# Kernel tuning notes

Measured on AMD Instinct MI355X. Metric: run time of the kernel, lower is better.

## Reference

```python
import jax, jax.numpy as jnp
import numpy as np

B, S, D = 2, 4096, 1024
H, HD = 16, 64
M = 512              # memseqlen == chunk size
L = 2 * M            # memory + chunk tokens
HID = 2816
EPS = 1e-5


def setup_inputs() -> dict:
    key = jax.random.key(0)
    ks = jax.random.split(key, 16)
    sc = 0.02
    return {
        "x": jax.random.normal(ks[0], (B, S, D), jnp.float32),
        "freqs_cos": jax.random.uniform(ks[1], (L, HD // 2), jnp.float32),
        "freqs_sin": jax.random.uniform(ks[2], (L, HD // 2), jnp.float32),
        "wq": jax.random.normal(ks[3], (D, D), jnp.float32) * sc,
        "wk": jax.random.normal(ks[4], (D, D), jnp.float32) * sc,
        "wv": jax.random.normal(ks[5], (D, D), jnp.float32) * sc,
        "wo": jax.random.normal(ks[6], (D, D), jnp.float32) * sc,
        "wm": jax.random.normal(ks[7], (D, D), jnp.float32) * sc,
        "wkm": jax.random.normal(ks[8], (D, D), jnp.float32) * sc,
        "wvm": jax.random.normal(ks[9], (D, D), jnp.float32) * sc,
        "w1": jax.random.normal(ks[10], (D, HID), jnp.float32) * sc,
        "w3": jax.random.normal(ks[11], (D, HID), jnp.float32) * sc,
        "w2": jax.random.normal(ks[12], (HID, D), jnp.float32) * sc,
        "ffn_norm_w": jnp.ones((D,), jnp.float32),
        "mem_norm_w": jnp.ones((D,), jnp.float32),
        "origin_mem": jnp.zeros((1, M, D), jnp.float32),
    }


def _rmsnorm(x, w):
    return x * jax.lax.rsqrt(jnp.mean(x * x, axis=-1, keepdims=True) + EPS) * w


def _rope(t, cos, sin):
    # t: (B, L, H, HD); cos/sin: (L, HD//2). Adjacent-pair complex rotation (llama2.c style).
    tr = t.reshape(*t.shape[:-1], HD // 2, 2)
    t_r, t_i = tr[..., 0], tr[..., 1]
    c = cos[None, :, None, :]
    s = sin[None, :, None, :]
    o_r = t_r * c - t_i * s
    o_i = t_r * s + t_i * c
    return jnp.stack([o_r, o_i], axis=-1).reshape(t.shape)


def reference(x, freqs_cos, freqs_sin, wq, wk, wv, wo, wm, wkm, wvm,
              w1, w2, w3, ffn_norm_w, mem_norm_w, origin_mem):
    bsz = x.shape[0]
    cos = freqs_cos[:L]
    sin = freqs_sin[:L]
    causal = jnp.tril(jnp.ones((L, L), dtype=bool))
    scale = 1.0 / jnp.sqrt(jnp.asarray(HD, x.dtype))

    def ffn(h):
        return (jax.nn.silu(h @ w1) * (h @ w3)) @ w2

    def step(om, subx):
        # token projections
        xq = (subx @ wq).reshape(bsz, M, H, HD)
        xk = (subx @ wk).reshape(bsz, M, H, HD)
        xv = (subx @ wv).reshape(bsz, M, H, HD)
        # memory glue: wm -> ffn residual -> rmsnorm
        om2 = om @ wm
        om2 = om2 + ffn(_rmsnorm(om2, ffn_norm_w))
        om2 = _rmsnorm(om2, mem_norm_w)
        # memory projections (source bug: mq is overwritten by mk; wqm unused)
        mk = (om2 @ wkm).reshape(bsz, M, H, HD)
        mv = (om2 @ wvm).reshape(bsz, M, H, HD)
        mq = mk
        q = jnp.concatenate([mq, xq], axis=1)  # (B, L, H, HD)
        k = jnp.concatenate([mk, xk], axis=1)
        v = jnp.concatenate([mv, xv], axis=1)
        q = _rope(q, cos, sin)
        k = _rope(k, cos, sin)
        # SDPA, causal over the concatenated length (n_rep == 1, repeat_kv is identity)
        qh = q.transpose(0, 2, 1, 3)
        kh = k.transpose(0, 2, 1, 3)
        vh = v.transpose(0, 2, 1, 3)
        scores = jnp.einsum('bhqd,bhkd->bhqk', qh, kh) * scale
        scores = jnp.where(causal, scores, jnp.finfo(scores.dtype).min)
        attn = jax.nn.softmax(scores, axis=-1)
        out = jnp.einsum('bhqk,bhkd->bhqd', attn, vh)
        out = out.transpose(0, 2, 1, 3).reshape(bsz, L, D)
        om_new = out[:, M:]  # token-part becomes next memory AND this chunk's output
        return om_new, om_new

    om0 = jnp.broadcast_to(origin_mem, (bsz, M, D))
    xc = x.reshape(bsz, S // M, M, D).transpose(1, 0, 2, 3)  # (n_chunks, B, M, D)
    _, outs = jax.lax.scan(step, om0, xc)
    out = outs.transpose(1, 0, 2, 3).reshape(bsz, S, D)
    return out @ wo
```

## Files before the change

kernel.cpp:

```cpp
#include <hip/hip_runtime.h>
#include <hip/hip_bf16.h>


#define D_    1024
#define H_    16
#define HD_   64
#define M_    512
#define L_    1024
#define HID_  2816
#define NSTEP 8

typedef __hip_bfloat16 bf16;
typedef _Float16 f16;
typedef __attribute__((ext_vector_type(8))) short short8;
typedef __attribute__((ext_vector_type(8))) _Float16 f16x8;
typedef __attribute__((ext_vector_type(4))) _Float16 f16x4;
typedef __attribute__((ext_vector_type(2))) _Float16 f16x2;
typedef __attribute__((ext_vector_type(4))) float floatx4;

__global__ void probe_dtype(const void* x, int* flag) {
  int lane = threadIdx.x;
  unsigned short v = ((const unsigned short*)x)[2 * lane];
  int e = (v >> 7) & 0xFF;
  bool sane = (e >= 100 && e <= 140);
  unsigned long long m = __ballot(sane);
  if (lane == 0) flag[0] = (__popcll(m) >= 40) ? 1 : 0;
}

__device__ __forceinline__ float load_any(const void* p, long i, int isbf) {
  return isbf ? __bfloat162float(((const bf16*)p)[i]) : ((const float*)p)[i];
}

__global__ __launch_bounds__(256) void transpose_cast(const void* in, bf16* out,
                                                      int K, int N, const int* flagp,
                                                      int stride, int off) {
  __shared__ float tile[32][33];
  int isbf = flagp[0];
  int tx = threadIdx.x & 31, ty = threadIdx.x >> 5;
  int n = blockIdx.x * 32 + tx;
#pragma unroll
  for (int i = 0; i < 4; i++) {
    int k = blockIdx.y * 32 + ty + i * 8;
    tile[ty + i * 8][tx] = load_any(in, (long)k * N + n, isbf);
  }
  __syncthreads();
  int k2 = blockIdx.y * 32 + tx;
#pragma unroll
  for (int i = 0; i < 4; i++) {
    int n2 = blockIdx.x * 32 + ty + i * 8;
    out[((long)n2 * stride + off) * K + k2] = __float2bfloat16(tile[tx][ty + i * 8]);
  }
}

__global__ __launch_bounds__(256) void cast_to_bf16(const void* in, bf16* out, int n,
                                                    const int* flagp) {
  int i = blockIdx.x * 256 + threadIdx.x;
  if (i < n) out[i] = __float2bfloat16(load_any(in, i, flagp[0]));
}

__global__ __launch_bounds__(256) void cast_to_f32(const void* in, float* out, int n,
                                                   const int* flagp) {
  int i = blockIdx.x * 256 + threadIdx.x;
  if (i < n) out[i] = load_any(in, i, flagp[0]);
}

__global__ __launch_bounds__(256) void init_om(const void* in, bf16* om, const int* flagp) {
  int i = blockIdx.x * 256 + threadIdx.x;
  int rem = i & (M_ * D_ - 1);
  om[i] = __float2bfloat16(load_any(in, rem, flagp[0]));
}

#define GEMM64_BODY(Aptr, WTptr, Kld, kbeg, kend)                                   \
  __shared__ char smem[16384];                                                      \
  char* aT = smem;                                                                  \
  char* bT = smem + 8192;                                                           \
  int tid = threadIdx.x;                                                            \
  int wave = tid >> 6, lane = tid & 63;                                             \
  int wm_ = wave >> 1, wn_ = wave & 1;                                              \
  floatx4 acc[2][2] = {};                                                           \
  int q0 = tid, q1 = tid + 256;                                                     \
  int am0 = q0 >> 3, ac0 = q0 & 7;                                                  \
  int am1 = q1 >> 3, ac1 = q1 & 7;                                                  \
  long grow0 = R0 + am0, grow1 = R0 + am1;                                          \
  long bn0 = (long)(C0 + am0) * (Kld), bn1 = (long)(C0 + am1) * (Kld);              \
  int lofa0 = (am0 * 8 + (ac0 ^ (am0 & 7))) * 16;                                   \
  int lofa1 = (am1 * 8 + (ac1 ^ (am1 & 7))) * 16;                                   \
  for (int k0 = (kbeg); k0 < (kend); k0 += 64) {                                    \
    uint4 va0 = *(const uint4*)((Aptr) + grow0 * (Kld) + k0 + ac0 * 8);             \
    uint4 va1 = *(const uint4*)((Aptr) + grow1 * (Kld) + k0 + ac1 * 8);             \
    uint4 vb0 = *(const uint4*)((WTptr) + bn0 + k0 + ac0 * 8);                      \
    uint4 vb1 = *(const uint4*)((WTptr) + bn1 + k0 + ac1 * 8);                      \
    __syncthreads();                                                                \
    *(uint4*)(aT + lofa0) = va0;                                                    \
    *(uint4*)(aT + lofa1) = va1;                                                    \
    *(uint4*)(bT + lofa0) = vb0;                                                    \
    *(uint4*)(bT + lofa1) = vb1;                                                    \
    __syncthreads();                                                                \
    _Pragma("unroll") for (int kki = 0; kki < 2; ++kki) {                           \
      int cbase = kki * 4 + (lane >> 4);                                            \
      short8 af[2], bfr[2];                                                         \
      _Pragma("unroll") for (int i = 0; i < 2; ++i) {                               \
        int ml = wm_ * 32 + i * 16 + (lane & 15);                                   \
        af[i] = *(const short8*)(aT + (ml * 8 + (cbase ^ (ml & 7))) * 16);          \
        int nl = wn_ * 32 + i * 16 + (lane & 15);                                   \
        bfr[i] = *(const short8*)(bT + (nl * 8 + (cbase ^ (nl & 7))) * 16);         \
      }                                                                             \
      _Pragma("unroll") for (int i = 0; i < 2; ++i)                                 \
          _Pragma("unroll") for (int j = 0; j < 2; ++j) acc[i][j] =                 \
              __builtin_amdgcn_mfma_f32_16x16x32_bf16(af[i], bfr[j], acc[i][j],     \
                                                      0, 0, 0);                     \
    }                                                                               \
  }

__global__ __launch_bounds__(256) void gemm64_sk(
    const bf16* __restrict__ A, const bf16* __restrict__ WT,
    float* __restrict__ outP, int N, int Kfull, int Ksplit) {
  int C0 = blockIdx.x * 64, R0 = blockIdx.y * 64;
  int kb = blockIdx.z;
  float* out = outP + ((size_t)kb << 20);
  int kbeg = kb * Ksplit;
  GEMM64_BODY(A, WT, Kfull, kbeg, kbeg + Ksplit)
#pragma unroll
  for (int i = 0; i < 2; ++i)
#pragma unroll
    for (int j = 0; j < 2; ++j) {
      int row = R0 + wm_ * 32 + i * 16 + (lane >> 4) * 4;
      int col = C0 + wn_ * 32 + j * 16 + (lane & 15);
#pragma unroll
      for (int rg = 0; rg < 4; ++rg)
        out[(long)(row + rg) * N + col] = acc[i][j][rg];
    }
}

__global__ __launch_bounds__(256) void gemm64_kmvm(
    const bf16* __restrict__ A, const bf16* __restrict__ WT,
    const float* __restrict__ cosf, const float* __restrict__ sinf,
    f16* __restrict__ k_mem, f16* __restrict__ v_memT) {
  int C0 = blockIdx.x * 64, R0 = blockIdx.y * 64;
  GEMM64_BODY(A, WT, 1024, 0, 1024)
#pragma unroll
  for (int i = 0; i < 2; ++i)
#pragma unroll
    for (int j = 0; j < 2; ++j) {
      int row0 = R0 + wm_ * 32 + i * 16 + (lane >> 4) * 4;
      int col = C0 + wn_ * 32 + j * 16 + (lane & 15);
#pragma unroll
      for (int rg = 0; rg < 4; ++rg) {
        float v = acc[i][j][rg];
        int row = row0 + rg;
        int b = row >> 9, pos = row & 511;
        if (C0 < 1024) {
          float partner = __shfl_xor(v, 1);
          int ii = (col & 63) >> 1;
          float c = cosf[pos * 32 + ii], s = sinf[pos * 32 + ii];
          float o = (col & 1) ? (partner * s + v * c) : (v * c - partner * s);
          int bh = b * 16 + ((col >> 6) & 15);
          k_mem[((size_t)bh * 512 + pos) * 64 + (col & 63)] = (f16)o;
        } else {
          int d = col & 63;
          int bh = b * 16 + ((col - 1024) >> 6);
          v_memT[((size_t)bh * 64 + d) * 512 + pos] = (f16)v;
        }
      }
    }
}

__global__ __launch_bounds__(256) void gemm128(
    const bf16* __restrict__ A, const bf16* __restrict__ WT,
    void* __restrict__ out, const int* __restrict__ flagp,
    int N, int K, int out_mode,
    const float* __restrict__ cosf, const float* __restrict__ sinf,
    f16* __restrict__ q_x, f16* __restrict__ k_x, f16* __restrict__ v_xT) {
  __shared__ char smem[32768];
  int tid = threadIdx.x;
  int w = tid >> 6, lane = tid & 63;
  int C0 = blockIdx.x * 128, R0 = blockIdx.y * 128;
  int wm = (w >> 1) * 64, wn = (w & 1) * 64;
  int g = lane >> 4, n16 = lane & 15;
  floatx4 acc[4][4] = {};
  int lr = lane >> 3, lc = lane & 7;

  for (int k0 = 0; k0 < K; k0 += 64) {
    __syncthreads();
#pragma unroll
    for (int i = 0; i < 4; ++i) {
      int m = w * 32 + i * 8 + lr;
      int cg = lc ^ (m & 7);
      const bf16* ga = A + (size_t)(R0 + m) * K + k0 + cg * 8;
      const bf16* gb = WT + (size_t)(C0 + m) * K + k0 + cg * 8;
      __builtin_amdgcn_global_load_lds(
          (const __attribute__((address_space(1))) void*)ga,
          (__attribute__((address_space(3))) void*)(smem + (w * 32 + i * 8) * 128),
          16, 0, 0);
      __builtin_amdgcn_global_load_lds(
          (const __attribute__((address_space(1))) void*)gb,
          (__attribute__((address_space(3))) void*)(smem + 16384 + (w * 32 + i * 8) * 128),
          16, 0, 0);
    }
    __syncthreads();
#pragma unroll
    for (int kk = 0; kk < 2; ++kk) {
      short8 af[4], bfr[4];
#pragma unroll
      for (int i = 0; i < 4; ++i) {
        int ml = wm + i * 16 + n16;
        af[i] = *(const short8*)(smem + (ml * 8 + ((kk * 4 + g) ^ (ml & 7))) * 16);
        int nl = wn + i * 16 + n16;
        bfr[i] = *(const short8*)(smem + 16384 + (nl * 8 + ((kk * 4 + g) ^ (nl & 7))) * 16);
      }
#pragma unroll
      for (int i = 0; i < 4; ++i)
#pragma unroll
        for (int j = 0; j < 4; ++j)
          acc[i][j] = __builtin_amdgcn_mfma_f32_16x16x32_bf16(af[i], bfr[j], acc[i][j], 0, 0, 0);
    }
  }
  int isbf = flagp ? flagp[0] : 0;
#pragma unroll
  for (int i = 0; i < 4; ++i)
#pragma unroll
    for (int j = 0; j < 4; ++j) {
      int row = R0 + wm + i * 16 + g * 4;
      int col = C0 + wn + j * 16 + n16;
      if (out_mode == 4) {
        if (col < 2048) {
#pragma unroll
          for (int rg = 0; rg < 4; ++rg) {
            float v = acc[i][j][rg];
            float partner = __shfl_xor(v, 1);
            int r = row + rg;
            int m = r & 511, t = (r >> 9) & 7, b = r >> 12;
            int pos = 512 + m;
            int ii = (col & 63) >> 1;
            float c = cosf[pos * 32 + ii], s = sinf[pos * 32 + ii];
            float o = (col & 1) ? (partner * s + v * c) : (v * c - partner * s);
            int h = (col >> 6) & 15;
            size_t slab = (size_t)t * 32 + b * 16 + h;
            if (col < 1024)
              q_x[(slab * 512 + m) * 64 + (col & 63)] = (f16)(o * 0.125f);
            else
              k_x[(slab * 512 + m) * 64 + (col & 63)] = (f16)o;
          }
        } else {
          int r = row;
          int m = r & 511, t = (r >> 9) & 7, b = r >> 12;
          int d = col & 63, h = (col - 2048) >> 6;
          size_t slab = (size_t)t * 32 + b * 16 + h;
          f16x4 vv;
#pragma unroll
          for (int rg = 0; rg < 4; ++rg) vv[rg] = (f16)acc[i][j][rg];
          *(f16x4*)(v_xT + (slab * 64 + d) * 512 + m) = vv;
        }
        continue;
      }
#pragma unroll
      for (int rg = 0; rg < 4; ++rg) {
        float v = acc[i][j][rg];
        if (out_mode == 3) {
          float partner = __shfl_xor(v, 1);
          if ((n16 & 1) == 0) {
            float a = v;
            float s = a / (1.f + __expf(-a));
            ((bf16*)out)[(long)(row + rg) * HID_ + (col >> 1)] =
                __float2bfloat16(s * partner);
          }
          continue;
        }
        long off = (long)(row + rg) * N + col;
        if (out_mode == 0) ((float*)out)[off] = v;
        else if (out_mode == 1) ((f16*)out)[off] = (f16)v;
        else {
          if (isbf) ((bf16*)out)[off] = __float2bfloat16(v);
          else ((float*)out)[off] = v;
        }
      }
    }
}

__global__ __launch_bounds__(256) void rmsnorm_cast(const float* __restrict__ X,
                                                    const float* __restrict__ Wn,
                                                    bf16* __restrict__ Y,
                                                    const float* __restrict__ P,
                                                    int np,
                                                    float* __restrict__ sumout) {
  int row = blockIdx.x, tid = threadIdx.x;
  float vals[4], ss = 0.f;
#pragma unroll
  for (int i = 0; i < 4; i++) {
    int c = tid + i * 256;
    long idx = (long)row * D_ + c;
    float v = X ? X[idx] : 0.f;
    for (int k = 0; k < np; ++k) v += P[((size_t)k << 20) + idx];
    vals[i] = v;
    ss += v * v;
  }
#pragma unroll
  for (int off = 32; off; off >>= 1) ss += __shfl_xor(ss, off);
  __shared__ float wsum[4];
  int wv = tid >> 6, lane = tid & 63;
  if (lane == 0) wsum[wv] = ss;
  __syncthreads();
  ss = wsum[0] + wsum[1] + wsum[2] + wsum[3];
  float r = rsqrtf(ss * (1.0f / D_) + 1e-5f);
#pragma unroll
  for (int i = 0; i < 4; i++) {
    int c = tid + i * 256;
    if (sumout) sumout[(long)row * D_ + c] = vals[i];
    Y[(long)row * D_ + c] = __float2bfloat16(vals[i] * r * Wn[c]);
  }
}

__global__ __launch_bounds__(256) void attn_mfma(
    const f16* __restrict__ q_x, const f16* __restrict__ k_mem,
    const f16* __restrict__ v_memT, const f16* __restrict__ k_x,
    const f16* __restrict__ v_xT, float* __restrict__ Opart,
    float* __restrict__ mpart, float* __restrict__ lpart, int t) {
  __shared__ char smem[24576];
  int qt = blockIdx.x, bh = blockIdx.y, z = blockIdx.z;
  int tid = threadIdx.x;
  int w = tid >> 6, lane = tid & 63;
  int g = lane >> 4, n16 = lane & 15;
  int c0 = z ? 8 : 0;
  int numc = z ? (qt + 1) : 8;
  int pos = 512 + qt * 64 + w * 16 + n16;
  size_t slab = (size_t)t * 32 + bh;

  f16x8 qf[2];
  {
    const f16* qp = q_x + (slab * 512 + qt * 64 + w * 16 + n16) * 64 + g * 8;
    qf[0] = *(const f16x8*)(qp);
    qf[1] = *(const f16x8*)(qp + 32);
  }
  floatx4 O[4] = {};
  float mrun = -1e30f, lrun = 0.f;

  int id0 = tid, id1 = tid + 256;
  int r0 = id0 >> 3, cc0 = id0 & 7;
  int r1 = id1 >> 3, cc1 = id1 & 7;
  int lof0 = ((r0 << 3) | (cc0 ^ (r0 & 7))) * 16;
  int lof1 = ((r1 << 3) | (cc1 ^ (r1 & 7))) * 16;

  auto kaddr = [&](int c, int r) -> const f16* {
    return (c < 8) ? k_mem + ((size_t)bh * 512 + c * 64 + r) * 64
                   : k_x + (slab * 512 + (c - 8) * 64 + r) * 64;
  };
  auto vaddr = [&](int c, int d) -> const f16* {
    return (c < 8) ? v_memT + ((size_t)bh * 64 + d) * 512 + c * 64
                   : v_xT + (slab * 64 + d) * 512 + (c - 8) * 64;
  };

  uint4 kv0 = *(const uint4*)(kaddr(c0, r0) + cc0 * 8);
  uint4 kv1 = *(const uint4*)(kaddr(c0, r1) + cc1 * 8);
  uint4 vv0 = *(const uint4*)(vaddr(c0, r0) + cc0 * 8);
  uint4 vv1 = *(const uint4*)(vaddr(c0, r1) + cc1 * 8);

  char* Pw = smem + 16384 + w * 2048;

  for (int c = 0; c < numc; ++c) {
    __syncthreads();
    *(uint4*)(smem + lof0) = kv0;
    *(uint4*)(smem + lof1) = kv1;
    *(uint4*)(smem + 8192 + lof0) = vv0;
    *(uint4*)(smem + 8192 + lof1) = vv1;
    if (c + 1 < numc) {
      kv0 = *(const uint4*)(kaddr(c0 + c + 1, r0) + cc0 * 8);
      kv1 = *(const uint4*)(kaddr(c0 + c + 1, r1) + cc1 * 8);
      vv0 = *(const uint4*)(vaddr(c0 + c + 1, r0) + cc0 * 8);
      vv1 = *(const uint4*)(vaddr(c0 + c + 1, r1) + cc1 * 8);
    }
    __syncthreads();

    floatx4 S[4] = {};
    __builtin_amdgcn_s_setprio(1);
#pragma unroll
    for (int kk = 0; kk < 2; ++kk) {
#pragma unroll
      for (int tn = 0; tn < 4; ++tn) {
        int row = tn * 16 + n16;
        f16x8 kf = *(const f16x8*)(smem + (((row << 3) | ((kk * 4 + g) ^ (row & 7))) * 16));
        S[tn] = __builtin_amdgcn_mfma_f32_16x16x32_f16(kf, qf[kk], S[tn], 0, 0, 0);
      }
    }
    __builtin_amdgcn_s_setprio(0);
    if (z == 1 && c == numc - 1) {
      int kb = 512 + qt * 64;
#pragma unroll
      for (int tn = 0; tn < 4; ++tn)
#pragma unroll
        for (int r = 0; r < 4; ++r) {
          int key = kb + tn * 16 + g * 4 + r;
          if (key > pos) S[tn][r] = -1e30f;
        }
    }
    float smax = -1e30f;
#pragma unroll
    for (int tn = 0; tn < 4; ++tn)
#pragma unroll
      for (int r = 0; r < 4; ++r) smax = fmaxf(smax, S[tn][r]);
    smax = fmaxf(smax, __shfl_xor(smax, 16));
    smax = fmaxf(smax, __shfl_xor(smax, 32));
    float newm = fmaxf(mrun, smax);
    float corr = __expf(mrun - newm);
    mrun = newm;
    float lsum = 0.f;
    f16 pv[16];
#pragma unroll
    for (int tn = 0; tn < 4; ++tn)
#pragma unroll
      for (int r = 0; r < 4; ++r) {
        float p = __expf(S[tn][r] - newm);
        lsum += p;
        pv[tn * 4 + r] = (f16)p;
      }
    lsum += __shfl_xor(lsum, 16);
    lsum += __shfl_xor(lsum, 32);
    lrun = lrun * corr + lsum;
    float cr[4];
#pragma unroll
    for (int r = 0; r < 4; ++r) cr[r] = __shfl(corr, g * 4 + r);
#pragma unroll
    for (int dt = 0; dt < 4; ++dt)
#pragma unroll
      for (int r = 0; r < 4; ++r) O[dt][r] *= cr[r];
#pragma unroll
    for (int tn = 0; tn < 4; ++tn)
#pragma unroll
      for (int r = 0; r < 4; ++r) {
        int kap = tn * 16 + g * 4 + r;
        *(f16*)(Pw + (((n16 << 3) | ((kap >> 3) ^ (n16 & 7))) * 16 + (kap & 7) * 2)) =
            pv[tn * 4 + r];
      }
    __builtin_amdgcn_s_setprio(1);
#pragma unroll
    for (int kk = 0; kk < 2; ++kk) {
      f16x8 pf = *(const f16x8*)(Pw + (((n16 << 3) | ((kk * 4 + g) ^ (n16 & 7))) * 16));
#pragma unroll
      for (int dt = 0; dt < 4; ++dt) {
        int row = dt * 16 + n16;
        f16x8 vf =
            *(const f16x8*)(smem + 8192 + (((row << 3) | ((kk * 4 + g) ^ (row & 7))) * 16));
        O[dt] = __builtin_amdgcn_mfma_f32_16x16x32_f16(pf, vf, O[dt], 0, 0, 0);
      }
    }
    __builtin_amdgcn_s_setprio(0);
  }
  int b = bh >> 4, h = bh & 15;
  if (g == 0) {
    int qq = qt * 64 + w * 16 + n16;
    mpart[(size_t)z * 16384 + bh * 512 + qq] = mrun;
    lpart[(size_t)z * 16384 + bh * 512 + qq] = lrun;
  }
#pragma unroll
  for (int dt = 0; dt < 4; ++dt)
#pragma unroll
    for (int r = 0; r < 4; ++r) {
      int qq = qt * 64 + w * 16 + g * 4 + r;
      size_t col = (size_t)h * 64 + dt * 16 + n16;
      Opart[(size_t)z * 1048576 + (size_t)(b * 512 + qq) * 1024 + col] = O[dt][r];
    }
}

__global__ __launch_bounds__(256) void attn_merge(
    const float* __restrict__ Opart, const float* __restrict__ mpart,
    const float* __restrict__ lpart, bf16* __restrict__ om_bf,
    bf16* __restrict__ outs_bf, int t) {
  int row = blockIdx.x;
  int b = row >> 9, qq = row & 511;
  int tid = threadIdx.x;
#pragma unroll
  for (int ii = 0; ii < 4; ++ii) {
    int col = tid + ii * 256;
    int bh = b * 16 + (col >> 6);
    int idx = bh * 512 + qq;
    float m1 = mpart[idx], l1 = lpart[idx];
    float m2 = mpart[16384 + idx], l2 = lpart[16384 + idx];
    float Mx = fmaxf(m1, m2);
    float a1 = __expf(m1 - Mx), a2 = __expf(m2 - Mx);
    float o1 = Opart[(size_t)row * 1024 + col];
    float o2 = Opart[1048576 + (size_t)row * 1024 + col];
    float v = (a1 * o1 + a2 * o2) / (a1 * l1 + a2 * l2);
    bf16 bv = __float2bfloat16(v);
    om_bf[(size_t)row * 1024 + col] = bv;
    outs_bf[((size_t)(b * 4096 + t * 512 + qq)) * 1024 + col] = bv;
  }
}

extern "C" void kernel_launch(void* const* d_in, const int* in_sizes, int n_in,
                              void* d_out, int out_size, void* d_ws, size_t ws_size,
                              hipStream_t stream) {
  (void)in_sizes; (void)n_in; (void)out_size; (void)ws_size;
  const void* x   = d_in[0];
  const void* fc  = d_in[1];
  const void* fs  = d_in[2];
  const void* wq  = d_in[3];
  const void* wk  = d_in[4];
  const void* wv  = d_in[5];
  const void* wo  = d_in[6];
  const void* wm  = d_in[7];
  const void* wkm = d_in[8];
  const void* wvm = d_in[9];
  const void* w1  = d_in[10];
  const void* w3  = d_in[11];
  const void* w2  = d_in[12];
  const void* fnw = d_in[13];
  const void* mnw = d_in[14];
  const void* om0 = d_in[15];

  char* p = (char*)d_ws;
  auto alloc = [&](size_t bytes) -> char* {
    char* r = p;
    p += (bytes + 255) & ~(size_t)255;
    return r;
  };
  int*   flag    = (int*)alloc(256);
  bf16*  wqkvT   = (bf16*)alloc((size_t)3 * 1048576 * 2);
  bf16*  wmT     = (bf16*)alloc((size_t)1048576 * 2);
  bf16*  wkmvmT  = (bf16*)alloc((size_t)2 * 1048576 * 2);
  bf16*  w13T    = (bf16*)alloc((size_t)2 * 2883584 * 2);
  bf16*  w2T     = (bf16*)alloc((size_t)2883584 * 2);
  bf16*  woT     = (bf16*)alloc((size_t)1048576 * 2);
  bf16*  xb      = (bf16*)alloc((size_t)8388608 * 2);
  float* cosf    = (float*)alloc((size_t)32768 * 4);
  float* sinf    = (float*)alloc((size_t)32768 * 4);
  float* ffnw    = (float*)alloc((size_t)1024 * 4);
  float* memw    = (float*)alloc((size_t)1024 * 4);
  bf16*  om_bf   = (bf16*)alloc((size_t)1048576 * 2);
  bf16*  outs_bf = (bf16*)alloc((size_t)8388608 * 2);
  f16*   q_x     = (f16*)alloc((size_t)8 * 32 * 512 * 64 * 2);
  f16*   k_x     = (f16*)alloc((size_t)8 * 32 * 512 * 64 * 2);
  f16*   v_xT    = (f16*)alloc((size_t)8 * 32 * 512 * 64 * 2);
  float* om2a   = (float*)alloc((size_t)1048576 * 4);
  bf16*  h_bf   = (bf16*)alloc((size_t)1048576 * 2);
  bf16*  u_bf   = (bf16*)alloc((size_t)2883584 * 2);
  float* om2P   = (float*)alloc((size_t)2 * 1048576 * 4);
  bf16*  om2_bf = (bf16*)alloc((size_t)1048576 * 2);
  f16*   k_mem  = (f16*)alloc((size_t)1048576 * 2);
  f16*   v_memT = (f16*)alloc((size_t)1048576 * 2);
  float* Opart  = (float*)alloc((size_t)2 * 1048576 * 4);
  float* mpart  = (float*)alloc((size_t)2 * 16384 * 4);
  float* lpart  = (float*)alloc((size_t)2 * 16384 * 4);

  dim3 tb(256);
  probe_dtype<<<1, 64, 0, stream>>>(x, flag);

  transpose_cast<<<dim3(32, 32), tb, 0, stream>>>(wq, wqkvT, 1024, 1024, flag, 1, 0);
  transpose_cast<<<dim3(32, 32), tb, 0, stream>>>(wk, wqkvT + 1048576, 1024, 1024, flag, 1, 0);
  transpose_cast<<<dim3(32, 32), tb, 0, stream>>>(wv, wqkvT + 2 * 1048576, 1024, 1024, flag, 1, 0);
  transpose_cast<<<dim3(32, 32), tb, 0, stream>>>(wm, wmT, 1024, 1024, flag, 1, 0);
  transpose_cast<<<dim3(32, 32), tb, 0, stream>>>(wkm, wkmvmT, 1024, 1024, flag, 1, 0);
  transpose_cast<<<dim3(32, 32), tb, 0, stream>>>(wvm, wkmvmT + 1048576, 1024, 1024, flag, 1, 0);
  transpose_cast<<<dim3(88, 32), tb, 0, stream>>>(w1, w13T, 1024, 2816, flag, 2, 0);
  transpose_cast<<<dim3(88, 32), tb, 0, stream>>>(w3, w13T, 1024, 2816, flag, 2, 1);
  transpose_cast<<<dim3(32, 88), tb, 0, stream>>>(w2, w2T, 2816, 1024, flag, 1, 0);
  transpose_cast<<<dim3(32, 32), tb, 0, stream>>>(wo, woT, 1024, 1024, flag, 1, 0);

  cast_to_bf16<<<32768, tb, 0, stream>>>(x, xb, 8388608, flag);
  cast_to_f32<<<128, tb, 0, stream>>>(fc, cosf, 32768, flag);
  cast_to_f32<<<128, tb, 0, stream>>>(fs, sinf, 32768, flag);
  cast_to_f32<<<4, tb, 0, stream>>>(fnw, ffnw, 1024, flag);
  cast_to_f32<<<4, tb, 0, stream>>>(mnw, memw, 1024, flag);
  init_om<<<4096, tb, 0, stream>>>(om0, om_bf, flag);

  gemm128<<<dim3(24, 64), tb, 0, stream>>>(xb, wqkvT, nullptr, flag, 3072, 1024, 4,
                                           cosf, sinf, q_x, k_x, v_xT);

  for (int t = 0; t < NSTEP; ++t) {
    gemm64_sk<<<dim3(16, 16, 2), tb, 0, stream>>>(om_bf, wmT, om2P, 1024, 1024, 512);
    rmsnorm_cast<<<1024, tb, 0, stream>>>(nullptr, ffnw, h_bf, om2P, 2, om2a);
    gemm128<<<dim3(44, 8), tb, 0, stream>>>(h_bf, w13T, u_bf, flag, 5632, 1024, 3,
                                            nullptr, nullptr, nullptr, nullptr, nullptr);
    gemm64_sk<<<dim3(16, 16, 2), tb, 0, stream>>>(u_bf, w2T, om2P, 1024, 2816, 1408);
    rmsnorm_cast<<<1024, tb, 0, stream>>>(om2a, memw, om2_bf, om2P, 2, nullptr);
    gemm64_kmvm<<<dim3(32, 16), tb, 0, stream>>>(om2_bf, wkmvmT, cosf, sinf, k_mem, v_memT);
    attn_mfma<<<dim3(8, 32, 2), tb, 0, stream>>>(q_x, k_mem, v_memT, k_x, v_xT,
                                                 Opart, mpart, lpart, t);
    attn_merge<<<1024, tb, 0, stream>>>(Opart, mpart, lpart, om_bf, outs_bf, t);
  }
  gemm128<<<dim3(8, 64), tb, 0, stream>>>(outs_bf, woT, d_out, flag, 1024, 1024, 2,
                                          nullptr, nullptr, nullptr, nullptr, nullptr);
}
```

Baseline: 1.132 ms.

## Double-buffer K/V tiles, lazy softmax rescale, vectorized P stores in attention

Splits the K/V LDS staging into two ping-pong buffers so one barrier per key chunk can be dropped. Softmax rescaling of the output accumulator now only happens when any row max grows by more than a threshold, skipping exp and multiply work otherwise. Probabilities are packed as f16x4 and stored with vector writes instead of scalar halves. LDS use rises, which may reduce occupancy, and deferring the rescale lets unnormalized values grow larger in f16.

```diff
diff --git a/kernel.cpp b/kernel.cpp
--- a/kernel.cpp
+++ b/kernel.cpp
@@ -315,7 +315,7 @@
     const f16* __restrict__ v_memT, const f16* __restrict__ k_x,
     const f16* __restrict__ v_xT, float* __restrict__ Opart,
     float* __restrict__ mpart, float* __restrict__ lpart, int t) {
-  __shared__ char smem[24576];
+  __shared__ char smem[40960];
   int qt = blockIdx.x, bh = blockIdx.y, z = blockIdx.z;
   int tid = threadIdx.x;
   int w = tid >> 6, lane = tid & 63;
@@ -354,14 +354,15 @@
   uint4 vv0 = *(const uint4*)(vaddr(c0, r0) + cc0 * 8);
   uint4 vv1 = *(const uint4*)(vaddr(c0, r1) + cc1 * 8);
 
-  char* Pw = smem + 16384 + w * 2048;
+  char* Pw = smem + 32768 + w * 2048;
 
   for (int c = 0; c < numc; ++c) {
-    __syncthreads();
-    *(uint4*)(smem + lof0) = kv0;
-    *(uint4*)(smem + lof1) = kv1;
-    *(uint4*)(smem + 8192 + lof0) = vv0;
-    *(uint4*)(smem + 8192 + lof1) = vv1;
+    char* Kb = smem + (c & 1) * 8192;
+    char* Vb = smem + 16384 + (c & 1) * 8192;
+    *(uint4*)(Kb + lof0) = kv0;
+    *(uint4*)(Kb + lof1) = kv1;
+    *(uint4*)(Vb + lof0) = vv0;
+    *(uint4*)(Vb + lof1) = vv1;
     if (c + 1 < numc) {
       kv0 = *(const uint4*)(kaddr(c0 + c + 1, r0) + cc0 * 8);
       kv1 = *(const uint4*)(kaddr(c0 + c + 1, r1) + cc1 * 8);
@@ -377,7 +378,7 @@
 #pragma unroll
       for (int tn = 0; tn < 4; ++tn) {
         int row = tn * 16 + n16;
-        f16x8 kf = *(const f16x8*)(smem + (((row << 3) | ((kk * 4 + g) ^ (row & 7))) * 16));
+        f16x8 kf = *(const f16x8*)(Kb + (((row << 3) | ((kk * 4 + g) ^ (row & 7))) * 16));
         S[tn] = __builtin_amdgcn_mfma_f32_16x16x32_f16(kf, qf[kk], S[tn], 0, 0, 0);
       }
     }
@@ -399,37 +400,35 @@
       for (int r = 0; r < 4; ++r) smax = fmaxf(smax, S[tn][r]);
     smax = fmaxf(smax, __shfl_xor(smax, 16));
     smax = fmaxf(smax, __shfl_xor(smax, 32));
-    float newm = fmaxf(mrun, smax);
-    float corr = __expf(mrun - newm);
-    mrun = newm;
+    float corr = 1.f;
+    if (__any(smax > mrun + 8.f)) {
+      float newm = fmaxf(mrun, smax);
+      corr = __expf(mrun - newm);
+      mrun = newm;
+      float cr[4];
+#pragma unroll
+      for (int r = 0; r < 4; ++r) cr[r] = __shfl(corr, g * 4 + r);
+#pragma unroll
+      for (int dt = 0; dt < 4; ++dt)
+#pragma unroll
+        for (int r = 0; r < 4; ++r) O[dt][r] *= cr[r];
+    }
     float lsum = 0.f;
-    f16 pv[16];
-#pragma unroll
-    for (int tn = 0; tn < 4; ++tn)
+#pragma unroll
+    for (int tn = 0; tn < 4; ++tn) {
+      f16x4 pk;
 #pragma unroll
       for (int r = 0; r < 4; ++r) {
-        float p = __expf(S[tn][r] - newm);
+        float p = __expf(S[tn][r] - mrun);
         lsum += p;
-        pv[tn * 4 + r] = (f16)p;
-      }
+        pk[r] = (f16)p;
+      }
+      int kapb = tn * 16 + g * 4;
+      *(f16x4*)(Pw + (((n16 << 3) | ((kapb >> 3) ^ (n16 & 7))) * 16 + (kapb & 7) * 2)) = pk;
+    }
     lsum += __shfl_xor(lsum, 16);
     lsum += __shfl_xor(lsum, 32);
     lrun = lrun * corr + lsum;
-    float cr[4];
-#pragma unroll
-    for (int r = 0; r < 4; ++r) cr[r] = __shfl(corr, g * 4 + r);
-#pragma unroll
-    for (int dt = 0; dt < 4; ++dt)
-#pragma unroll
-      for (int r = 0; r < 4; ++r) O[dt][r] *= cr[r];
-#pragma unroll
-    for (int tn = 0; tn < 4; ++tn)
-#pragma unroll
-      for (int r = 0; r < 4; ++r) {
-        int kap = tn * 16 + g * 4 + r;
-        *(f16*)(Pw + (((n16 << 3) | ((kap >> 3) ^ (n16 & 7))) * 16 + (kap & 7) * 2)) =
-            pv[tn * 4 + r];
-      }
     __builtin_amdgcn_s_setprio(1);
 #pragma unroll
     for (int kk = 0; kk < 2; ++kk) {
@@ -438,7 +437,7 @@
       for (int dt = 0; dt < 4; ++dt) {
         int row = dt * 16 + n16;
         f16x8 vf =
-            *(const f16x8*)(smem + 8192 + (((row << 3) | ((kk * 4 + g) ^ (row & 7))) * 16));
+            *(const f16x8*)(Vb + (((row << 3) | ((kk * 4 + g) ^ (row & 7))) * 16));
         O[dt] = __builtin_amdgcn_mfma_f32_16x16x32_f16(pf, vf, O[dt], 0, 0, 0);
       }
     }
```

Result: no change. 1.125 ms (-0.6%).
